# Optimization experiments

Measured on AMD Instinct MI355X. Metric: run time of the kernel, lower is better.

Reference implementation:

```python
import jax, jax.numpy as jnp
import numpy as np

H, W = 1024, 1024
K = 15            # degree_max / neighbour_nb
GAMMA = 0.5
MULTIPLIER = 1.0
WIN = 4           # half window for neighbor offsets (window_size=9)


def setup_inputs() -> dict:
    key = jax.random.key(0)
    k1, k2, k3, k4, k5 = jax.random.split(key, 5)
    N = H * W
    sig1 = jax.random.normal(k1, (1, 1, H, W), dtype=jnp.float32)
    sig2 = jax.random.normal(k2, (1, 2, H, W), dtype=jnp.float32)
    weights = jax.random.uniform(k3, (K, N), dtype=jnp.float32)
    # Build a local-window neighbor graph, as similarity_graph would produce.
    idx = jnp.arange(N, dtype=jnp.int32)
    y = idx // W
    x = idx % W
    dy = jax.random.randint(k4, (K, N), -WIN, WIN + 1, dtype=jnp.int32)
    dx = jax.random.randint(k5, (K, N), -WIN, WIN + 1, dtype=jnp.int32)
    yn = jnp.clip(y[None] + dy, 0, H - 1)
    xn = jnp.clip(x[None] + dx, 0, W - 1)
    neighbours = (yn * W + xn).astype(jnp.int32)            # (K, N)
    # dist = (x_source - x_target, y_source - y_target), per constructor.
    dist = jnp.stack([(x[None] - xn), (y[None] - yn)], axis=1).astype(jnp.float32)  # (K, 2, N)
    return {"sig1": sig1, "sig2": sig2, "weights": weights, "dist": dist,
            "neighbours": neighbours}


def reference(sig1, sig2, weights, dist, neighbours):
    N = weights.shape[1]
    s1 = sig1.reshape(-1)                 # (N,)
    s2 = sig2.reshape(2, -1)              # (2, N)
    # planar term: sum_c sig2[c, n] * dist[k, c, n]  -> (K, N)
    plane = jnp.einsum('cn,kcn->kn', s2, dist)
    aux1 = s1[None, :] - s1[neighbours] - plane           # (K, N)
    aux1 = jnp.sqrt(jnp.sum((aux1 * weights) ** 2, axis=0)).sum()
    # vector-field difference: (K, 2, N), norm over channel dim
    diff2 = s2[None, :, :] - jnp.transpose(s2[:, neighbours], (1, 0, 2))
    aux2 = jnp.sqrt(jnp.sum(diff2 * diff2, axis=1))        # (K, N)
    aux2 = jnp.sum(aux2 * weights)
    loss = (aux1 + GAMMA * aux2) / N
    return MULTIPLIER * loss
```

## Files before the change

kernel.cpp:

```cpp
#include <hip/hip_runtime.h>
#include <hip/hip_bf16.h>

#define HH 1024
#define WW 1024
#define NN (HH * WW)
#define KK 15
#define GAMMA_F 0.5f

#define TR 12
#define TW 72

__device__ __forceinline__ void cp16(const float* g, float* l) {
    __builtin_amdgcn_global_load_lds(
        (const __attribute__((address_space(1))) void*)g,
        (__attribute__((address_space(3))) void*)l, 16, 0, 0);
}

__global__ __launch_bounds__(256) void ppr_kernel(
    const float* __restrict__ s1,
    const float* __restrict__ s2,
    const float* __restrict__ w,
    const int* __restrict__ nb,
    float* __restrict__ out)
{
    __shared__ __align__(16) float t1 [TR * TW];
    __shared__ __align__(16) float t2a[TR * TW];
    __shared__ __align__(16) float t2b[TR * TW];
    __shared__ float smem[4];

    const int tid  = threadIdx.x;
    const int wv   = tid >> 6;
    const int lane = tid & 63;
    const int ty   = blockIdx.x >> 4;
    const int tx   = blockIdx.x & 15;
    const int y0   = ty << 2;
    const int c0   = tx << 6;
    const int yc   = y0 + wv;
    const int xc   = c0 + lane;
    const int n    = yc * WW + xc;

    int   j[KK];
    float wk[KK];
#pragma unroll
    for (int k = 0; k < KK; ++k) j[k]  = nb[(size_t)k * NN + n];
#pragma unroll
    for (int k = 0; k < KK; ++k) wk[k] = w[(size_t)k * NN + n];

    int xs = c0 - 4, dof = 0, nl = 18;
    if (tx == 0)       { xs = 0; dof = 4; nl = 17; }
    else if (tx == 15) { nl = 17; }

    for (int t = wv; t < 36; t += 4) {
        const int arr = t / 12;
        const int rr  = t - arr * 12;
        int gy = y0 - 4 + rr;
        gy = gy < 0 ? 0 : (gy > HH - 1 ? HH - 1 : gy);
        const float* src =
            (arr == 0 ? s1 : (arr == 1 ? s2 : s2 + NN)) + (size_t)gy * WW + xs;
        float* dst =
            (arr == 0 ? t1 : (arr == 1 ? t2a : t2b)) + rr * TW + dof;
        if (lane < nl) cp16(src + lane * 4, dst);
    }

    __builtin_amdgcn_sched_barrier(0);
    __syncthreads();

    const int own = (wv + 4) * TW + lane + 4;
    const float s1n = t1[own];
    const float s2a = t2a[own];
    const float s2b = t2b[own];

    const int cbase = (4 - y0) * TW + 4 - c0;

    float acc1 = 0.0f, acc2 = 0.0f;
#pragma unroll
    for (int k = 0; k < KK; ++k) {
        const int jj = j[k];
        const int yn = jj >> 10;
        const int xn = jj & (WW - 1);
        const int off = yn * TW + xn + cbase;
        const float g1  = t1[off];
        const float g2a = t2a[off];
        const float g2b = t2b[off];

        const float d0 = (float)(xc - xn);
        const float d1 = (float)(yc - yn);

        const float plane = fmaf(s2a, d0, s2b * d1);
        const float a1 = (s1n - g1 - plane) * wk[k];
        acc1 = fmaf(a1, a1, acc1);

        const float e0 = s2a - g2a;
        const float e1 = s2b - g2b;
        acc2 = fmaf(sqrtf(fmaf(e0, e0, e1 * e1)), wk[k], acc2);
    }
    float local = sqrtf(acc1) + GAMMA_F * acc2;

#pragma unroll
    for (int off2 = 32; off2 > 0; off2 >>= 1)
        local += __shfl_down(local, off2, 64);

    if (lane == 0) smem[wv] = local;
    __syncthreads();

    if (tid == 0) {
        const float s = smem[0] + smem[1] + smem[2] + smem[3];
        atomicAdd(out, s * (1.0f / (float)NN));
    }
}

extern "C" void kernel_launch(void* const* d_in, const int* in_sizes, int n_in,
                              void* d_out, int out_size, void* d_ws, size_t ws_size,
                              hipStream_t stream) {
    const float* s1   = (const float*)d_in[0];
    const float* s2   = (const float*)d_in[1];
    const float* w    = (const float*)d_in[2];
    const int*   nb   = (const int*)d_in[4];
    float* out = (float*)d_out;

    hipMemsetAsync(out, 0, sizeof(float) * (size_t)out_size, stream);

    const int block = 256;
    const int grid  = NN / block;
    ppr_kernel<<<grid, block, 0, stream>>>(s1, s2, w, nb, out);
}
```

Measured before the change: 261.8 us.

## Process two pixels per thread with wider tiles and vectorized loads

Each thread now handles two adjacent pixels, so the tile width grows from 64 to 128 columns and the grid halves. Neighbour indices and weights are read as int2/float2 vector loads. The wider tile cuts the relative halo overhead and the number of atomics, and the fixed-count staging loop is unrolled. The cost is doubled per-thread register use (30 int2/float2 values) and fewer blocks, which may reduce occupancy and latency hiding.

```diff
diff --git a/kernel.cpp b/kernel.cpp
--- a/kernel.cpp
+++ b/kernel.cpp
@@ -8,7 +8,7 @@
 #define GAMMA_F 0.5f
 
 #define TR 12
-#define TW 72
+#define TW 136
 
 __device__ __forceinline__ void cp16(const float* g, float* l) {
     __builtin_amdgcn_global_load_lds(
@@ -31,70 +31,90 @@
     const int tid  = threadIdx.x;
     const int wv   = tid >> 6;
     const int lane = tid & 63;
-    const int ty   = blockIdx.x >> 4;
-    const int tx   = blockIdx.x & 15;
+    const int ty   = blockIdx.x >> 3;
+    const int tx   = blockIdx.x & 7;
     const int y0   = ty << 2;
-    const int c0   = tx << 6;
+    const int c0   = tx << 7;
     const int yc   = y0 + wv;
-    const int xc   = c0 + lane;
-    const int n    = yc * WW + xc;
+    const int xc0  = c0 + (lane << 1);
+    const int n    = yc * WW + xc0;
 
-    int   j[KK];
-    float wk[KK];
+    int2   j2[KK];
+    float2 w2[KK];
 #pragma unroll
-    for (int k = 0; k < KK; ++k) j[k]  = nb[(size_t)k * NN + n];
+    for (int k = 0; k < KK; ++k) j2[k] = *(const int2*)(nb + (size_t)k * NN + n);
 #pragma unroll
-    for (int k = 0; k < KK; ++k) wk[k] = w[(size_t)k * NN + n];
+    for (int k = 0; k < KK; ++k) w2[k] = *(const float2*)(w + (size_t)k * NN + n);
 
-    int xs = c0 - 4, dof = 0, nl = 18;
-    if (tx == 0)       { xs = 0; dof = 4; nl = 17; }
-    else if (tx == 15) { nl = 17; }
+    int xs = c0 - 4, dof = 0, nl = 34;
+    if (tx == 0)      { xs = 0; dof = 4; nl = 33; }
+    else if (tx == 7) { nl = 33; }
 
-    for (int t = wv; t < 36; t += 4) {
+#pragma unroll
+    for (int it = 0; it < 9; ++it) {
+        const int t   = wv * 9 + it;
         const int arr = t / 12;
         const int rr  = t - arr * 12;
         int gy = y0 - 4 + rr;
         gy = gy < 0 ? 0 : (gy > HH - 1 ? HH - 1 : gy);
         const float* src =
             (arr == 0 ? s1 : (arr == 1 ? s2 : s2 + NN)) + (size_t)gy * WW + xs;
-        float* dst =
-            (arr == 0 ? t1 : (arr == 1 ? t2a : t2b)) + rr * TW + dof;
+        float* dst = (arr == 0 ? t1 : (arr == 1 ? t2a : t2b)) + rr * TW + dof;
         if (lane < nl) cp16(src + lane * 4, dst);
     }
 
     __builtin_amdgcn_sched_barrier(0);
     __syncthreads();
 
-    const int own = (wv + 4) * TW + lane + 4;
-    const float s1n = t1[own];
-    const float s2a = t2a[own];
-    const float s2b = t2b[own];
+    const int own0 = (wv + 4) * TW + (lane << 1) + 4;
+    const float s1n_0 = t1 [own0],     s1n_1 = t1 [own0 + 1];
+    const float s2a_0 = t2a[own0],     s2a_1 = t2a[own0 + 1];
+    const float s2b_0 = t2b[own0],     s2b_1 = t2b[own0 + 1];
 
     const int cbase = (4 - y0) * TW + 4 - c0;
 
-    float acc1 = 0.0f, acc2 = 0.0f;
+    float acc1_0 = 0.f, acc2_0 = 0.f, acc1_1 = 0.f, acc2_1 = 0.f;
 #pragma unroll
     for (int k = 0; k < KK; ++k) {
-        const int jj = j[k];
-        const int yn = jj >> 10;
-        const int xn = jj & (WW - 1);
-        const int off = yn * TW + xn + cbase;
-        const float g1  = t1[off];
-        const float g2a = t2a[off];
-        const float g2b = t2b[off];
-
-        const float d0 = (float)(xc - xn);
-        const float d1 = (float)(yc - yn);
-
-        const float plane = fmaf(s2a, d0, s2b * d1);
-        const float a1 = (s1n - g1 - plane) * wk[k];
-        acc1 = fmaf(a1, a1, acc1);
-
-        const float e0 = s2a - g2a;
-        const float e1 = s2b - g2b;
-        acc2 = fmaf(sqrtf(fmaf(e0, e0, e1 * e1)), wk[k], acc2);
+        {
+            const int jj = j2[k].x;
+            const int yn = jj >> 10;
+            const int xn = jj & (WW - 1);
+            const int off = yn * TW + xn + cbase;
+            const float g1  = t1 [off];
+            const float g2a = t2a[off];
+            const float g2b = t2b[off];
+            const float d0 = (float)(xc0 - xn);
+            const float d1 = (float)(yc  - yn);
+            const float wkk = w2[k].x;
+            const float plane = fmaf(s2a_0, d0, s2b_0 * d1);
+            const float a1 = (s1n_0 - g1 - plane) * wkk;
+            acc1_0 = fmaf(a1, a1, acc1_0);
+            const float e0 = s2a_0 - g2a;
+            const float e1 = s2b_0 - g2b;
+            acc2_0 = fmaf(sqrtf(fmaf(e0, e0, e1 * e1)), wkk, acc2_0);
+        }
+        {
+            const int jj = j2[k].y;
+            const int yn = jj >> 10;
+            const int xn = jj & (WW - 1);
+            const int off = yn * TW + xn + cbase;
+            const float g1  = t1 [off];
+            const float g2a = t2a[off];
+            const float g2b = t2b[off];
+            const float d0 = (float)(xc0 + 1 - xn);
+            const float d1 = (float)(yc - yn);
+            const float wkk = w2[k].y;
+            const float plane = fmaf(s2a_1, d0, s2b_1 * d1);
+            const float a1 = (s1n_1 - g1 - plane) * wkk;
+            acc1_1 = fmaf(a1, a1, acc1_1);
+            const float e0 = s2a_1 - g2a;
+            const float e1 = s2b_1 - g2b;
+            acc2_1 = fmaf(sqrtf(fmaf(e0, e0, e1 * e1)), wkk, acc2_1);
+        }
     }
-    float local = sqrtf(acc1) + GAMMA_F * acc2;
+    float local = sqrtf(acc1_0) + sqrtf(acc1_1)
+                + GAMMA_F * (acc2_0 + acc2_1);
 
 #pragma unroll
     for (int off2 = 32; off2 > 0; off2 >>= 1)
@@ -121,6 +141,6 @@
     hipMemsetAsync(out, 0, sizeof(float) * (size_t)out_size, stream);
 
     const int block = 256;
-    const int grid  = NN / block;
+    const int grid  = NN / (block * 2);
     ppr_kernel<<<grid, block, 0, stream>>>(s1, s2, w, nb, out);
 }
```

Result: faster. 248.0 us (-5.3%).

## Process four pixels per thread with vectorized loads and wider LDS tiles

Applied to the files above, without the earlier changes.

Each thread now handles four consecutive pixels, loading neighbour indices and weights as int4/float4, and each block covers a 256-wide strip with a 264-wide LDS halo tile. This cuts the grid by four and reduces halo overhead and per-load instruction count. The planar term is algebraically split into a per-pixel constant plus a per-neighbour part, and half the index/weight loads are issued before the barrier to overlap with the tile copy. The cost is higher register pressure (60 index/weight values per thread) and fewer blocks, which may lower occupancy.

```diff
diff --git a/kernel.cpp b/kernel.cpp
--- a/kernel.cpp
+++ b/kernel.cpp
@@ -8,7 +8,7 @@
 #define GAMMA_F 0.5f
 
 #define TR 12
-#define TW 72
+#define TW 264
 
 __device__ __forceinline__ void cp16(const float* g, float* l) {
     __builtin_amdgcn_global_load_lds(
@@ -31,70 +31,97 @@
     const int tid  = threadIdx.x;
     const int wv   = tid >> 6;
     const int lane = tid & 63;
-    const int ty   = blockIdx.x >> 4;
-    const int tx   = blockIdx.x & 15;
+    const int ty   = blockIdx.x >> 2;
+    const int tx   = blockIdx.x & 3;
     const int y0   = ty << 2;
-    const int c0   = tx << 6;
+    const int c0   = tx << 8;
     const int yc   = y0 + wv;
-    const int xc   = c0 + lane;
-    const int n    = yc * WW + xc;
+    const int xc0  = c0 + (lane << 2);
+    const int n    = (yc << 10) + xc0;
+    const int t4   = n >> 2;
 
-    int   j[KK];
-    float wk[KK];
+    const int mainXs  = (tx == 0) ? 0   : c0 - 4;
+    const int mainDof = (tx == 0) ? 4   : 0;
+    const int tailXs  = (tx == 0) ? 256 : c0 + 252;
+    const int tailDof = (tx == 0) ? 260 : 256;
+    const int tailLn  = (tx == 0 || tx == 3) ? 1 : 2;
+
 #pragma unroll
-    for (int k = 0; k < KK; ++k) j[k]  = nb[(size_t)k * NN + n];
-#pragma unroll
-    for (int k = 0; k < KK; ++k) wk[k] = w[(size_t)k * NN + n];
-
-    int xs = c0 - 4, dof = 0, nl = 18;
-    if (tx == 0)       { xs = 0; dof = 4; nl = 17; }
-    else if (tx == 15) { nl = 17; }
-
-    for (int t = wv; t < 36; t += 4) {
+    for (int it = 0; it < 9; ++it) {
+        const int t   = wv * 9 + it;
         const int arr = t / 12;
         const int rr  = t - arr * 12;
         int gy = y0 - 4 + rr;
         gy = gy < 0 ? 0 : (gy > HH - 1 ? HH - 1 : gy);
         const float* src =
-            (arr == 0 ? s1 : (arr == 1 ? s2 : s2 + NN)) + (size_t)gy * WW + xs;
-        float* dst =
-            (arr == 0 ? t1 : (arr == 1 ? t2a : t2b)) + rr * TW + dof;
-        if (lane < nl) cp16(src + lane * 4, dst);
+            (arr == 0 ? s1 : (arr == 1 ? s2 : s2 + NN)) + (size_t)gy * WW;
+        float* dst = (arr == 0 ? t1 : (arr == 1 ? t2a : t2b)) + rr * TW;
+        cp16(src + mainXs + lane * 4, dst + mainDof);
+        if (lane < tailLn) cp16(src + tailXs + lane * 4, dst + tailDof);
     }
+
+    int4   j4[KK];
+    float4 w4[KK];
+#pragma unroll
+    for (int k = 0; k < 8; ++k) j4[k] = ((const int4*)(nb + (size_t)k * NN))[t4];
+#pragma unroll
+    for (int k = 0; k < 8; ++k) w4[k] = ((const float4*)(w + (size_t)k * NN))[t4];
 
     __builtin_amdgcn_sched_barrier(0);
     __syncthreads();
 
-    const int own = (wv + 4) * TW + lane + 4;
-    const float s1n = t1[own];
-    const float s2a = t2a[own];
-    const float s2b = t2b[own];
+#pragma unroll
+    for (int k = 8; k < KK; ++k) j4[k] = ((const int4*)(nb + (size_t)k * NN))[t4];
+#pragma unroll
+    for (int k = 8; k < KK; ++k) w4[k] = ((const float4*)(w + (size_t)k * NN))[t4];
+    __builtin_amdgcn_sched_barrier(0);
+
+    const int own = (wv + 4) * TW + (lane << 2) + 4;
+    const float4 s14 = *(const float4*)(t1  + own);
+    const float4 sa4 = *(const float4*)(t2a + own);
+    const float4 sb4 = *(const float4*)(t2b + own);
+    const float s1n[4] = { s14.x, s14.y, s14.z, s14.w };
+    const float sa [4] = { sa4.x, sa4.y, sa4.z, sa4.w };
+    const float sb [4] = { sb4.x, sb4.y, sb4.z, sb4.w };
+
+    const float ycf = (float)yc;
+    float D[4];
+#pragma unroll
+    for (int i = 0; i < 4; ++i)
+        D[i] = s1n[i] - fmaf(sa[i], (float)(xc0 + i), sb[i] * ycf);
 
     const int cbase = (4 - y0) * TW + 4 - c0;
 
-    float acc1 = 0.0f, acc2 = 0.0f;
+    float acc1[4] = {0.f, 0.f, 0.f, 0.f};
+    float acc2[4] = {0.f, 0.f, 0.f, 0.f};
 #pragma unroll
     for (int k = 0; k < KK; ++k) {
-        const int jj = j[k];
-        const int yn = jj >> 10;
-        const int xn = jj & (WW - 1);
-        const int off = yn * TW + xn + cbase;
-        const float g1  = t1[off];
-        const float g2a = t2a[off];
-        const float g2b = t2b[off];
+        const int   jjs[4] = { j4[k].x, j4[k].y, j4[k].z, j4[k].w };
+        const float wks[4] = { w4[k].x, w4[k].y, w4[k].z, w4[k].w };
+#pragma unroll
+        for (int i = 0; i < 4; ++i) {
+            const unsigned jj = (unsigned)jjs[i];
+            const int yn = jj >> 10;
+            const int xn = jj & (WW - 1);
+            const int off = yn * TW + xn + cbase;
+            const float g1  = t1 [off];
+            const float g2a = t2a[off];
+            const float g2b = t2b[off];
 
-        const float d0 = (float)(xc - xn);
-        const float d1 = (float)(yc - yn);
+            const float P  = fmaf(sa[i], (float)xn, sb[i] * (float)yn);
+            const float a1 = (D[i] + (P - g1)) * wks[i];
+            acc1[i] = fmaf(a1, a1, acc1[i]);
 
-        const float plane = fmaf(s2a, d0, s2b * d1);
-        const float a1 = (s1n - g1 - plane) * wk[k];
-        acc1 = fmaf(a1, a1, acc1);
+            const float e0 = sa[i] - g2a;
+            const float e1 = sb[i] - g2b;
+            acc2[i] = fmaf(sqrtf(fmaf(e0, e0, e1 * e1)), wks[i], acc2[i]);
+        }
+    }
 
-        const float e0 = s2a - g2a;
-        const float e1 = s2b - g2b;
-        acc2 = fmaf(sqrtf(fmaf(e0, e0, e1 * e1)), wk[k], acc2);
-    }
-    float local = sqrtf(acc1) + GAMMA_F * acc2;
+    float local = 0.0f;
+#pragma unroll
+    for (int i = 0; i < 4; ++i)
+        local += sqrtf(acc1[i]) + GAMMA_F * acc2[i];
 
 #pragma unroll
     for (int off2 = 32; off2 > 0; off2 >>= 1)
@@ -121,6 +148,6 @@
     hipMemsetAsync(out, 0, sizeof(float) * (size_t)out_size, stream);
 
     const int block = 256;
-    const int grid  = NN / block;
+    const int grid  = NN / (block * 4);
     ppr_kernel<<<grid, block, 0, stream>>>(s1, s2, w, nb, out);
 }
```

After: 259.1 us. No clear change (-1.0%).

## Make blocks persistent over four tiles with double-buffered LDS prefetch

Applied to the files above, without the earlier changes.

Each block now processes four consecutive 4x64 tiles. It double-buffers the LDS halo tiles and the per-thread neighbour and weight registers, so the next tile's global loads are issued before the current tile is computed. The aim is to hide global-memory latency and amortise per-block setup and the final atomic over more work. The plane term is also rewritten algebraically, with a per-pixel constant hoisted out of the k loop. In exchange the grid is four times smaller and register pressure roughly doubles, which can lower occupancy. Reassociating the subtraction may also shift float rounding slightly.

```diff
diff --git a/kernel.cpp b/kernel.cpp
--- a/kernel.cpp
+++ b/kernel.cpp
@@ -9,6 +9,7 @@
 
 #define TR 12
 #define TW 72
+#define TPB 4
 
 __device__ __forceinline__ void cp16(const float* g, float* l) {
     __builtin_amdgcn_global_load_lds(
@@ -23,78 +24,93 @@
     const int* __restrict__ nb,
     float* __restrict__ out)
 {
-    __shared__ __align__(16) float t1 [TR * TW];
-    __shared__ __align__(16) float t2a[TR * TW];
-    __shared__ __align__(16) float t2b[TR * TW];
+    __shared__ __align__(16) float t1 [2][TR * TW];
+    __shared__ __align__(16) float t2a[2][TR * TW];
+    __shared__ __align__(16) float t2b[2][TR * TW];
     __shared__ float smem[4];
 
     const int tid  = threadIdx.x;
     const int wv   = tid >> 6;
     const int lane = tid & 63;
-    const int ty   = blockIdx.x >> 4;
-    const int tx   = blockIdx.x & 15;
-    const int y0   = ty << 2;
-    const int c0   = tx << 6;
-    const int yc   = y0 + wv;
-    const int xc   = c0 + lane;
-    const int n    = yc * WW + xc;
+    const int tile0 = blockIdx.x * TPB;
 
-    int   j[KK];
-    float wk[KK];
+    int   jj [2][KK];
+    float wk2[2][KK];
+    float local = 0.0f;
+
+    auto issue_tile = [&](int tile, int buf) {
+        const int ty = tile >> 4, tx = tile & 15;
+        const int y0 = ty << 2,  c0 = tx << 6;
+        const int n  = ((y0 + wv) << 10) + c0 + lane;
+
 #pragma unroll
-    for (int k = 0; k < KK; ++k) j[k]  = nb[(size_t)k * NN + n];
+        for (int k = 0; k < KK; ++k) jj[buf][k]  = nb[(size_t)k * NN + n];
 #pragma unroll
-    for (int k = 0; k < KK; ++k) wk[k] = w[(size_t)k * NN + n];
+        for (int k = 0; k < KK; ++k) wk2[buf][k] = w[(size_t)k * NN + n];
 
-    int xs = c0 - 4, dof = 0, nl = 18;
-    if (tx == 0)       { xs = 0; dof = 4; nl = 17; }
-    else if (tx == 15) { nl = 17; }
+        int xs = c0 - 4, dof = 0, nl = 18;
+        if (tx == 0)       { xs = 0; dof = 4; nl = 17; }
+        else if (tx == 15) { nl = 17; }
 
-    for (int t = wv; t < 36; t += 4) {
-        const int arr = t / 12;
-        const int rr  = t - arr * 12;
-        int gy = y0 - 4 + rr;
-        gy = gy < 0 ? 0 : (gy > HH - 1 ? HH - 1 : gy);
-        const float* src =
-            (arr == 0 ? s1 : (arr == 1 ? s2 : s2 + NN)) + (size_t)gy * WW + xs;
-        float* dst =
-            (arr == 0 ? t1 : (arr == 1 ? t2a : t2b)) + rr * TW + dof;
-        if (lane < nl) cp16(src + lane * 4, dst);
+#pragma unroll
+        for (int it = 0; it < 9; ++it) {
+            const int t   = wv * 9 + it;
+            const int arr = t / 12;
+            const int rr  = t - arr * 12;
+            int gy = y0 - 4 + rr;
+            gy = gy < 0 ? 0 : (gy > HH - 1 ? HH - 1 : gy);
+            const float* src =
+                (arr == 0 ? s1 : (arr == 1 ? s2 : s2 + NN)) + (size_t)gy * WW + xs;
+            float* dst =
+                (arr == 0 ? t1[buf] : (arr == 1 ? t2a[buf] : t2b[buf]))
+                + rr * TW + dof;
+            if (lane < nl) cp16(src + lane * 4, dst);
+        }
+    };
+
+    auto compute_tile = [&](int tile, int buf) {
+        const int ty = tile >> 4, tx = tile & 15;
+        const int y0 = ty << 2,  c0 = tx << 6;
+        const int yc = y0 + wv,  xc = c0 + lane;
+
+        const int own = (wv + 4) * TW + lane + 4;
+        const float s1n = t1[buf][own];
+        const float sa  = t2a[buf][own];
+        const float sb  = t2b[buf][own];
+        const float D = s1n - fmaf(sa, (float)xc, sb * (float)yc);
+        const int cbase = (4 - y0) * TW + 4 - c0;
+
+        float acc1 = 0.0f, acc2 = 0.0f;
+#pragma unroll
+        for (int k = 0; k < KK; ++k) {
+            const unsigned j = (unsigned)jj[buf][k];
+            const float  wkk = wk2[buf][k];
+            const int yn = j >> 10;
+            const int xn = j & (WW - 1);
+            const int off = yn * TW + xn + cbase;
+            const float g1  = t1 [buf][off];
+            const float g2a = t2a[buf][off];
+            const float g2b = t2b[buf][off];
+
+            const float P  = fmaf(sa, (float)xn, sb * (float)yn);
+            const float a1 = (D + (P - g1)) * wkk;
+            acc1 = fmaf(a1, a1, acc1);
+
+            const float e0 = sa - g2a;
+            const float e1 = sb - g2b;
+            acc2 = fmaf(sqrtf(fmaf(e0, e0, e1 * e1)), wkk, acc2);
+        }
+        local += sqrtf(acc1) + GAMMA_F * acc2;
+    };
+
+    issue_tile(tile0, 0);
+#pragma unroll
+    for (int t = 0; t < TPB; ++t) {
+        __syncthreads();
+        if (t + 1 < TPB) issue_tile(tile0 + t + 1, (t + 1) & 1);
+        __builtin_amdgcn_sched_barrier(0);
+        compute_tile(tile0 + t, t & 1);
     }
-
-    __builtin_amdgcn_sched_barrier(0);
-    __syncthreads();
-
-    const int own = (wv + 4) * TW + lane + 4;
-    const float s1n = t1[own];
-    const float s2a = t2a[own];
-    const float s2b = t2b[own];
-
-    const int cbase = (4 - y0) * TW + 4 - c0;
-
-    float acc1 = 0.0f, acc2 = 0.0f;
-#pragma unroll
-    for (int k = 0; k < KK; ++k) {
-        const int jj = j[k];
-        const int yn = jj >> 10;
-        const int xn = jj & (WW - 1);
-        const int off = yn * TW + xn + cbase;
-        const float g1  = t1[off];
-        const float g2a = t2a[off];
-        const float g2b = t2b[off];
-
-        const float d0 = (float)(xc - xn);
-        const float d1 = (float)(yc - yn);
-
-        const float plane = fmaf(s2a, d0, s2b * d1);
-        const float a1 = (s1n - g1 - plane) * wk[k];
-        acc1 = fmaf(a1, a1, acc1);
-
-        const float e0 = s2a - g2a;
-        const float e1 = s2b - g2b;
-        acc2 = fmaf(sqrtf(fmaf(e0, e0, e1 * e1)), wk[k], acc2);
-    }
-    float local = sqrtf(acc1) + GAMMA_F * acc2;
 
 #pragma unroll
     for (int off2 = 32; off2 > 0; off2 >>= 1)
@@ -121,6 +137,6 @@
     hipMemsetAsync(out, 0, sizeof(float) * (size_t)out_size, stream);
 
     const int block = 256;
-    const int grid  = NN / block;
+    const int grid  = NN / (block * TPB);
     ppr_kernel<<<grid, block, 0, stream>>>(s1, s2, w, nb, out);
 }
```

After: 254.6 us. 1.03x faster.
